# Optimization experiments

Hardware: AMD Instinct MI355X
Metric: run time of the kernel (lower is better)

## Reference

```python
import jax, jax.numpy as jnp
import numpy as np

EMBED_DIM = 512
NUM_HEADS = 8
HEAD_DIM = EMBED_DIM // NUM_HEADS
ATTN_STD = 1.0          # attn_param for attn_type='normal'
# attn_position='center' => no displacement of query indices


def setup_inputs() -> dict:
    key = jax.random.key(0)
    k1, k2, k3 = jax.random.split(key, 3)
    B, S = 4, 4096
    inputs = jax.random.normal(k1, (B, S, EMBED_DIM), dtype=jnp.float32)
    # xavier-uniform-like scale for [E, E] weights
    bound = np.float32(np.sqrt(6.0 / (EMBED_DIM + EMBED_DIM)))
    input_weights = jax.random.uniform(k2, (EMBED_DIM, EMBED_DIM), jnp.float32, -bound, bound)
    output_weight = jax.random.uniform(k3, (EMBED_DIM, EMBED_DIM), jnp.float32, -bound, bound)
    return {"inputs": inputs, "input_weights": input_weights, "output_weight": output_weight}


def _gaussian_weights(s_q, s_v, dtype):
    # logits[i, j] = 1/(std*sqrt(2*pi)) * exp(-0.5*((j-i)/std)^2)
    iq = jnp.arange(s_q, dtype=dtype)[:, None]
    iv = jnp.arange(s_v, dtype=dtype)[None, :]
    diff = iv - iq
    coef = (1.0 / (ATTN_STD * np.sqrt(2.0 * np.pi))).astype(np.float32)
    return coef * jnp.exp(-0.5 * (diff / ATTN_STD) ** 2)


def reference(inputs, input_weights, output_weight):
    B, S, E = inputs.shape
    H, D = NUM_HEADS, HEAD_DIM
    # project(): F.linear(inputs, input_weights) then split heads -> [B*H, S, D]
    v = jnp.einsum('bse,fe->bsf', inputs, input_weights)
    v = v.reshape(B, S, H, D).transpose(0, 2, 1, 3).reshape(B * H, S, D)
    # hard-coded Gaussian positional attention weights [S, S] (data independent)
    w = _gaussian_weights(S, S, inputs.dtype).astype(v.dtype)
    attended = jnp.einsum('qk,nkd->nqd', w, v)  # bmm with broadcast weights
    attended = attended.reshape(B, H, S, D).transpose(0, 2, 1, 3).reshape(B, S, E)
    # output_projection: Linear(E, E, bias=False)
    return jnp.einsum('bse,fe->bsf', attended, output_weight)
```

## Files before the change

### kernel.cpp

```cpp
#include <hip/hip_runtime.h>
#include <hip/hip_bf16.h>


typedef unsigned short u16;
typedef unsigned int u32;
typedef unsigned long long u64;
typedef __attribute__((ext_vector_type(8))) short bf16x8;
typedef __attribute__((ext_vector_type(8))) unsigned short u16x8;
typedef __attribute__((ext_vector_type(4))) float f32x4;
typedef __attribute__((ext_vector_type(2))) u32 u32x2;

typedef __attribute__((address_space(1))) const void* as1_cvp;
typedef __attribute__((address_space(3))) void* as3_vp;

#define EDIM 512
#define NROW 16384
#define NCONVB 4096
#define GOUT 512

__device__ __forceinline__ float b2f(u16 x) {
  union { u32 u; float f; } c; c.u = ((u32)x) << 16; return c.f;
}
__device__ __forceinline__ u16 f2b(float x) {
  union { float f; u32 u; } c; c.f = x;
  return (u16)((c.u + 0x7fffu + ((c.u >> 16) & 1u)) >> 16);
}
__device__ __forceinline__ u32 cvtpk(float lo, float hi) {
  u32 r;
  asm("v_cvt_pk_bf16_f32 %0, %1, %2" : "=v"(r) : "v"(lo), "v"(hi));
  return r;
}
__device__ __forceinline__ void async_cp16(const void* g, void* l) {
  __builtin_amdgcn_global_load_lds((as1_cvp)(u64)g, (as3_vp)(u32)(u64)l, 16, 0, 0);
}

__global__ __launch_bounds__(256) void prep(const float* __restrict__ in,
                                            const float* __restrict__ Win,
                                            const float* __restrict__ Wout,
                                            u16* __restrict__ Mm,
                                            u16* __restrict__ Uo) {
  __shared__ u16 plds[17408];
  int bid = (int)blockIdx.x, t = threadIdx.x;
  if (bid < 64) {
    u16* la = plds;
    u16* lbt = plds + 8704;
    int w = t >> 6, l = t & 63, lr = l & 15, lk = l >> 4;
    int f0 = (bid >> 3) * 64, e0 = (bid & 7) * 64;
    int arow = t >> 2, acol = (t & 3) * 32;
    int cq = t >> 3, eo = (t & 7) * 8;
    const float* pA = Wout + (u64)(f0 + arow) * EDIM + acol;
    const float* pB = Win + (u64)(4 * cq) * EDIM + e0 + eo;
    f32x4 a8[8], b8[8];
#pragma unroll
    for (int i = 0; i < 8; ++i) a8[i] = *(const f32x4*)(pA + i * 4);
#pragma unroll
    for (int r = 0; r < 4; ++r) {
      b8[r * 2 + 0] = *(const f32x4*)(pB + r * EDIM);
      b8[r * 2 + 1] = *(const f32x4*)(pB + r * EDIM + 4);
    }
    f32x4 acc[4] = {};
    for (int kt = 0; kt < 4; ++kt) {
#pragma unroll
      for (int i = 0; i < 4; ++i) {
        u16x8 o;
#pragma unroll
        for (int q = 0; q < 4; ++q) { o[q] = f2b(a8[2 * i][q]); o[4 + q] = f2b(a8[2 * i + 1][q]); }
        *(u16x8*)(la + arow * 136 + acol + i * 8) = o;
      }
#pragma unroll
      for (int j = 0; j < 8; ++j) {
        u32x2 p;
        p[0] = cvtpk(b8[0 + (j >> 2)][j & 3], b8[2 + (j >> 2)][j & 3]);
        p[1] = cvtpk(b8[4 + (j >> 2)][j & 3], b8[6 + (j >> 2)][j & 3]);
        *(u32x2*)(lbt + (eo + j) * 136 + 4 * cq) = p;
      }
      asm volatile("s_waitcnt lgkmcnt(0)" ::: "memory");
      __builtin_amdgcn_sched_barrier(0);
      __builtin_amdgcn_s_barrier();
      if (kt < 3) {
        pA += 128; pB += (u64)128 * EDIM;
#pragma unroll
        for (int i = 0; i < 8; ++i) a8[i] = *(const f32x4*)(pA + i * 4);
#pragma unroll
        for (int r = 0; r < 4; ++r) {
          b8[r * 2 + 0] = *(const f32x4*)(pB + r * EDIM);
          b8[r * 2 + 1] = *(const f32x4*)(pB + r * EDIM + 4);
        }
      }
#pragma unroll
      for (int kk = 0; kk < 128; kk += 32) {
        bf16x8 a = *(const bf16x8*)(la + (w * 16 + lr) * 136 + kk + lk * 8);
#pragma unroll
        for (int ni = 0; ni < 4; ++ni) {
          bf16x8 bb = *(const bf16x8*)(lbt + (ni * 16 + lr) * 136 + kk + lk * 8);
          acc[ni] = __builtin_amdgcn_mfma_f32_16x16x32_bf16(a, bb, acc[ni], 0, 0, 0);
        }
      }
      asm volatile("s_waitcnt lgkmcnt(0)" ::: "memory");
      __builtin_amdgcn_sched_barrier(0);
      __builtin_amdgcn_s_barrier();
    }
#pragma unroll
    for (int ni = 0; ni < 4; ++ni)
#pragma unroll
      for (int r = 0; r < 4; ++r)
        Mm[(u64)(f0 + w * 16 + lk * 4 + r) * EDIM + e0 + ni * 16 + lr] = f2b(acc[ni][r]);
  } else {
    const float G[5] = {0.39894228040143270f, 0.24197072451914337f,
                        0.053990966513188063f, 0.0044318484119380075f,
                        1.3383022576488537e-4f};
    int gid = (bid - 64) * 256 + t;
    int r = gid >> 6, c = (gid & 63) * 8;
    int s = r & 4095;
    const float* base = in + (u64)r * EDIM + c;
    float a[8] = {0.f, 0.f, 0.f, 0.f, 0.f, 0.f, 0.f, 0.f};
#pragma unroll
    for (int d = -4; d <= 4; ++d) {
      if ((unsigned)(s + d) < 4096u) {
        f32x4 v0 = *(const f32x4*)(base + (long)d * EDIM);
        f32x4 v1 = *(const f32x4*)(base + (long)d * EDIM + 4);
        float g = G[d < 0 ? -d : d];
#pragma unroll
        for (int q = 0; q < 4; ++q) { a[q] += g * v0[q]; a[4 + q] += g * v1[q]; }
      }
    }
    u16x8 o;
#pragma unroll
    for (int q = 0; q < 8; ++q) o[q] = f2b(a[q]);
    *(u16x8*)(Uo + (u64)r * EDIM + c) = o;
  }
}

__global__ __launch_bounds__(256) void gemm_out(const u16* __restrict__ U,
                                                const u16* __restrict__ Mm,
                                                float* __restrict__ out) {
  __shared__ u16 lds[32768];
  int t = threadIdx.x;
  int l = t & 63, lr = l & 15, lk = l >> 4;
  int wv = t >> 6, wr = wv >> 1, wc = wv & 1;
  int b = (int)blockIdx.x;
  int wg = (b & 7) * 64 + (b >> 3);
  int m0 = (wg >> 2) * 128;
  int n0 = (wg & 3) * 128;

  int soct = (t & 7) ^ ((t >> 3) & 7);
  const u16* gA = U + (u64)(m0 + (t >> 3)) * EDIM + soct * 8;
  const u16* gB = Mm + (u64)(n0 + (t >> 3)) * EDIM + soct * 8;

  int ard[4], aswz[4], brd[4], bswz[4];
#pragma unroll
  for (int mi = 0; mi < 4; ++mi) {
    int rA = wr * 64 + mi * 16 + lr;
    ard[mi] = rA * 64; aswz[mi] = (rA & 7) << 3;
  }
#pragma unroll
  for (int ni = 0; ni < 4; ++ni) {
    int rB = wc * 64 + ni * 16 + lr;
    brd[ni] = rB * 64; bswz[ni] = (rB & 7) << 3;
  }

  f32x4 acc[4][4] = {};

#pragma unroll
  for (int i = 0; i < 4; ++i) async_cp16(gA + (u64)i * 32 * EDIM, lds + t * 8 + i * 2048);
#pragma unroll
  for (int i = 0; i < 4; ++i) async_cp16(gB + (u64)i * 32 * EDIM, lds + 16384 + t * 8 + i * 2048);

#pragma unroll
  for (int kt = 0; kt < 8; ++kt) {
    asm volatile("s_waitcnt vmcnt(0)" ::: "memory");
    __builtin_amdgcn_sched_barrier(0);
    __builtin_amdgcn_s_barrier();
    if (kt < 7) {
      int ko = (kt + 1) * 64;
      int ab = ((kt + 1) & 1) * 8192, bb = 16384 + ((kt + 1) & 1) * 8192;
#pragma unroll
      for (int i = 0; i < 4; ++i) async_cp16(gA + ko + (u64)i * 32 * EDIM, lds + ab + t * 8 + i * 2048);
#pragma unroll
      for (int i = 0; i < 4; ++i) async_cp16(gB + ko + (u64)i * 32 * EDIM, lds + bb + t * 8 + i * 2048);
    }
    __builtin_amdgcn_sched_barrier(0);
    int ab = (kt & 1) * 8192, bb = 16384 + (kt & 1) * 8192;
#pragma unroll
    for (int kk = 0; kk < 64; kk += 32) {
      bf16x8 af[4], bv[4];
#pragma unroll
      for (int mi = 0; mi < 4; ++mi)
        af[mi] = *(const bf16x8*)(lds + ab + ard[mi] + ((kk + lk * 8) ^ aswz[mi]));
#pragma unroll
      for (int ni = 0; ni < 4; ++ni)
        bv[ni] = *(const bf16x8*)(lds + bb + brd[ni] + ((kk + lk * 8) ^ bswz[ni]));
#pragma unroll
      for (int mi = 0; mi < 4; ++mi)
#pragma unroll
        for (int ni = 0; ni < 4; ++ni)
          acc[mi][ni] = __builtin_amdgcn_mfma_f32_16x16x32_bf16(af[mi], bv[ni],
                                                                acc[mi][ni], 0, 0, 0);
    }
  }

#pragma unroll
  for (int mi = 0; mi < 4; ++mi)
#pragma unroll
    for (int ni = 0; ni < 4; ++ni)
#pragma unroll
      for (int rr = 0; rr < 4; ++rr)
        out[(u64)(m0 + wr * 64 + mi * 16 + lk * 4 + rr) * EDIM +
            n0 + wc * 64 + ni * 16 + lr] = acc[mi][ni][rr];
}

extern "C" void kernel_launch(void* const* d_in, const int* in_sizes, int n_in,
                              void* d_out, int out_size, void* d_ws, size_t ws_size,
                              hipStream_t stream) {
  const float* in   = (const float*)d_in[0];
  const float* Win  = (const float*)d_in[1];
  const float* Wout = (const float*)d_in[2];
  float* outp = (float*)d_out;

  u16* Mm = (u16*)d_ws;
  u16* Uo = (u16*)d_ws + (u64)EDIM * EDIM;

  hipLaunchKernelGGL(prep,     dim3(64 + NCONVB), dim3(256), 0, stream, in, Win, Wout, Mm, Uo);
  hipLaunchKernelGGL(gemm_out, dim3(GOUT),        dim3(256), 0, stream, Uo, Mm, outp);
}
```

Baseline: 39.89 us.

## Fuse Gaussian convolution into output GEMM A-tile loading

Removes the separate convolution pass that wrote a bf16 intermediate U to workspace. The GEMM kernel now loads fp32 input rows (a 16-row halo per 8-row group), applies the 9-tap Gaussian in registers and writes the A tile to LDS, prefetching the next K slice during the MFMA work. The combined-weight GEMM becomes its own small kernel. The intermediate write and read go away, but each of the four N-column blocks re-reads fp32 input with halo redundancy and does more VALU work, and it adds register pressure under launch_bounds(256,2).

```diff
diff --git a/kernel.cpp b/kernel.cpp
--- a/kernel.cpp
+++ b/kernel.cpp
@@ -15,12 +15,7 @@
 
 #define EDIM 512
 #define NROW 16384
-#define NCONVB 4096
-#define GOUT 512
-
-__device__ __forceinline__ float b2f(u16 x) {
-  union { u32 u; float f; } c; c.u = ((u32)x) << 16; return c.f;
-}
+
 __device__ __forceinline__ u16 f2b(float x) {
   union { float f; u32 u; } c; c.f = x;
   return (u16)((c.u + 0x7fffu + ((c.u >> 16) & 1u)) >> 16);
@@ -34,179 +29,221 @@
   __builtin_amdgcn_global_load_lds((as1_cvp)(u64)g, (as3_vp)(u32)(u64)l, 16, 0, 0);
 }
 
-__global__ __launch_bounds__(256) void prep(const float* __restrict__ in,
-                                            const float* __restrict__ Win,
-                                            const float* __restrict__ Wout,
-                                            u16* __restrict__ Mm,
-                                            u16* __restrict__ Uo) {
+__global__ __launch_bounds__(256) void gemm_m(const float* __restrict__ Wout,
+                                              const float* __restrict__ Win,
+                                              u16* __restrict__ Mm) {
   __shared__ u16 plds[17408];
-  int bid = (int)blockIdx.x, t = threadIdx.x;
-  if (bid < 64) {
-    u16* la = plds;
-    u16* lbt = plds + 8704;
-    int w = t >> 6, l = t & 63, lr = l & 15, lk = l >> 4;
-    int f0 = (bid >> 3) * 64, e0 = (bid & 7) * 64;
-    int arow = t >> 2, acol = (t & 3) * 32;
-    int cq = t >> 3, eo = (t & 7) * 8;
-    const float* pA = Wout + (u64)(f0 + arow) * EDIM + acol;
-    const float* pB = Win + (u64)(4 * cq) * EDIM + e0 + eo;
-    f32x4 a8[8], b8[8];
-#pragma unroll
-    for (int i = 0; i < 8; ++i) a8[i] = *(const f32x4*)(pA + i * 4);
-#pragma unroll
-    for (int r = 0; r < 4; ++r) {
-      b8[r * 2 + 0] = *(const f32x4*)(pB + r * EDIM);
-      b8[r * 2 + 1] = *(const f32x4*)(pB + r * EDIM + 4);
-    }
-    f32x4 acc[4] = {};
-    for (int kt = 0; kt < 4; ++kt) {
-#pragma unroll
-      for (int i = 0; i < 4; ++i) {
-        u16x8 o;
-#pragma unroll
-        for (int q = 0; q < 4; ++q) { o[q] = f2b(a8[2 * i][q]); o[4 + q] = f2b(a8[2 * i + 1][q]); }
-        *(u16x8*)(la + arow * 136 + acol + i * 8) = o;
-      }
-#pragma unroll
-      for (int j = 0; j < 8; ++j) {
-        u32x2 p;
-        p[0] = cvtpk(b8[0 + (j >> 2)][j & 3], b8[2 + (j >> 2)][j & 3]);
-        p[1] = cvtpk(b8[4 + (j >> 2)][j & 3], b8[6 + (j >> 2)][j & 3]);
-        *(u32x2*)(lbt + (eo + j) * 136 + 4 * cq) = p;
-      }
+  int t = threadIdx.x;
+  u16* la = plds;
+  u16* lbt = plds + 8704;
+  int w = t >> 6, l = t & 63, lr = l & 15, lk = l >> 4;
+  int f0 = ((int)blockIdx.x >> 3) * 64, e0 = ((int)blockIdx.x & 7) * 64;
+  int arow = t >> 2, acol = (t & 3) * 32;
+  int cq = t >> 3, eo = (t & 7) * 8;
+  const float* pA = Wout + (u64)(f0 + arow) * EDIM + acol;
+  const float* pB = Win + (u64)(4 * cq) * EDIM + e0 + eo;
+  f32x4 a8[8], b8[8];
+#pragma unroll
+  for (int i = 0; i < 8; ++i) a8[i] = *(const f32x4*)(pA + i * 4);
+#pragma unroll
+  for (int r = 0; r < 4; ++r) {
+    b8[r * 2 + 0] = *(const f32x4*)(pB + r * EDIM);
+    b8[r * 2 + 1] = *(const f32x4*)(pB + r * EDIM + 4);
+  }
+  f32x4 acc[4] = {};
+  for (int kt = 0; kt < 4; ++kt) {
+#pragma unroll
+    for (int i = 0; i < 4; ++i) {
+      u16x8 o;
+#pragma unroll
+      for (int q = 0; q < 4; ++q) { o[q] = f2b(a8[2 * i][q]); o[4 + q] = f2b(a8[2 * i + 1][q]); }
+      *(u16x8*)(la + arow * 136 + acol + i * 8) = o;
+    }
+#pragma unroll
+    for (int j = 0; j < 8; ++j) {
+      u32x2 p;
+      p[0] = cvtpk(b8[0 + (j >> 2)][j & 3], b8[2 + (j >> 2)][j & 3]);
+      p[1] = cvtpk(b8[4 + (j >> 2)][j & 3], b8[6 + (j >> 2)][j & 3]);
+      *(u32x2*)(lbt + (eo + j) * 136 + 4 * cq) = p;
+    }
+    asm volatile("s_waitcnt lgkmcnt(0)" ::: "memory");
+    __builtin_amdgcn_sched_barrier(0);
+    __builtin_amdgcn_s_barrier();
+    if (kt < 3) {
+      pA += 128; pB += (u64)128 * EDIM;
+#pragma unroll
+      for (int i = 0; i < 8; ++i) a8[i] = *(const f32x4*)(pA + i * 4);
+#pragma unroll
+      for (int r = 0; r < 4; ++r) {
+        b8[r * 2 + 0] = *(const f32x4*)(pB + r * EDIM);
+        b8[r * 2 + 1] = *(const f32x4*)(pB + r * EDIM + 4);
+      }
+    }
+#pragma unroll
+    for (int kk = 0; kk < 128; kk += 32) {
+      bf16x8 a = *(const bf16x8*)(la + (w * 16 + lr) * 136 + kk + lk * 8);
+#pragma unroll
+      for (int ni = 0; ni < 4; ++ni) {
+        bf16x8 bb = *(const bf16x8*)(lbt + (ni * 16 + lr) * 136 + kk + lk * 8);
+        acc[ni] = __builtin_amdgcn_mfma_f32_16x16x32_bf16(a, bb, acc[ni], 0, 0, 0);
+      }
+    }
+    asm volatile("s_waitcnt lgkmcnt(0)" ::: "memory");
+    __builtin_amdgcn_sched_barrier(0);
+    __builtin_amdgcn_s_barrier();
+  }
+#pragma unroll
+  for (int ni = 0; ni < 4; ++ni)
+#pragma unroll
+    for (int r = 0; r < 4; ++r)
+      Mm[(u64)(f0 + w * 16 + lk * 4 + r) * EDIM + e0 + ni * 16 + lr] = f2b(acc[ni][r]);
+}
+
+template <bool EDGE>
+__device__ __forceinline__ void conv_to_lds(u16* lds, int abase, const f32x4* w,
+                                            int r0, int tg, int ct, const float* G) {
+#pragma unroll
+  for (int j = 0; j < 8; ++j) {
+    f32x4 o = {};
+    if (EDGE) {
+      int rj = r0 + j, bat = rj >> 12;
+#pragma unroll
+      for (int k = 0; k < 9; ++k) {
+        float g = (((rj + k - 4) >> 12) == bat) ? G[k < 4 ? 4 - k : k - 4] : 0.0f;
+#pragma unroll
+        for (int q = 0; q < 4; ++q) o[q] += g * w[j + k][q];
+      }
+    } else {
+#pragma unroll
+      for (int k = 0; k < 9; ++k) {
+        float g = G[k < 4 ? 4 - k : k - 4];
+#pragma unroll
+        for (int q = 0; q < 4; ++q) o[q] += g * w[j + k][q];
+      }
+    }
+    int row = tg * 8 + j;
+    u32x2 p;
+    p[0] = cvtpk(o[0], o[1]);
+    p[1] = cvtpk(o[2], o[3]);
+    *(u32x2*)(lds + abase + ((row * 64 + ct * 4) ^ ((row & 7) << 3))) = p;
+  }
+}
+
+template <bool EDGE>
+__device__ __forceinline__ void fused_body(const float* __restrict__ in,
+                                           const u16* __restrict__ Mm,
+                                           float* __restrict__ out,
+                                           u16* lds, int t, int m0, int n0) {
+  const float G[5] = {0.39894228040143270f, 0.24197072451914337f,
+                      0.053990966513188063f, 0.0044318484119380075f,
+                      1.3383022576488537e-4f};
+  int l = t & 63, lr = l & 15, lk = l >> 4;
+  int wvi = t >> 6, wr = wvi >> 1, wc = wvi & 1;
+  int ct = t & 15, tg = t >> 4;
+  int r0 = m0 + tg * 8;
+
+  u32 woff[16];
+#pragma unroll
+  for (int i = 0; i < 16; ++i) {
+    int rr = r0 - 4 + i;
+    rr = rr < 0 ? 0 : (rr > NROW - 1 ? NROW - 1 : rr);
+    woff[i] = (u32)rr * EDIM + ct * 4;
+  }
+  int soct = (t & 7) ^ ((t >> 3) & 7);
+  const u16* gB = Mm + (u64)(n0 + (t >> 3)) * EDIM + soct * 8;
+
+  int ard[4], aswz[4], brd[4], bswz[4];
+#pragma unroll
+  for (int mi = 0; mi < 4; ++mi) {
+    int rA = wr * 64 + mi * 16 + lr;
+    ard[mi] = rA * 64; aswz[mi] = (rA & 7) << 3;
+  }
+#pragma unroll
+  for (int ni = 0; ni < 4; ++ni) {
+    int rB = wc * 64 + ni * 16 + lr;
+    brd[ni] = rB * 64; bswz[ni] = (rB & 7) << 3;
+  }
+
+  f32x4 acc[4][4] = {};
+  f32x4 w[16];
+
+#pragma unroll
+  for (int i = 0; i < 16; ++i) w[i] = *(const f32x4*)(in + woff[i]);
+  conv_to_lds<EDGE>(lds, 0, w, r0, tg, ct, G);
+#pragma unroll
+  for (int i = 0; i < 4; ++i)
+    async_cp16(gB + (u64)i * 32 * EDIM, lds + 16384 + t * 8 + i * 2048);
+  asm volatile("s_waitcnt lgkmcnt(0)" ::: "memory");
+  __builtin_amdgcn_sched_barrier(0);
+
+#pragma unroll
+  for (int kt = 0; kt < 8; ++kt) {
+    asm volatile("s_waitcnt vmcnt(0)" ::: "memory");
+    __builtin_amdgcn_sched_barrier(0);
+    __builtin_amdgcn_s_barrier();
+    if (kt < 7) {
+#pragma unroll
+      for (int i = 0; i < 16; ++i)
+        w[i] = *(const f32x4*)(in + woff[i] + (kt + 1) * 64);
+    }
+    __builtin_amdgcn_sched_barrier(0);
+    if (kt < 7) {
+#pragma unroll
+      for (int i = 0; i < 4; ++i)
+        async_cp16(gB + (kt + 1) * 64 + (u64)i * 32 * EDIM,
+                   lds + 16384 + ((kt + 1) & 1) * 8192 + t * 8 + i * 2048);
+    }
+    __builtin_amdgcn_sched_barrier(0);
+    int ab = (kt & 1) * 8192, bb = 16384 + (kt & 1) * 8192;
+#pragma unroll
+    for (int kk = 0; kk < 64; kk += 32) {
+      bf16x8 af[4], bv[4];
+#pragma unroll
+      for (int mi = 0; mi < 4; ++mi)
+        af[mi] = *(const bf16x8*)(lds + ab + ard[mi] + ((kk + lk * 8) ^ aswz[mi]));
+#pragma unroll
+      for (int ni = 0; ni < 4; ++ni)
+        bv[ni] = *(const bf16x8*)(lds + bb + brd[ni] + ((kk + lk * 8) ^ bswz[ni]));
+#pragma unroll
+      for (int mi = 0; mi < 4; ++mi)
+#pragma unroll
+        for (int ni = 0; ni < 4; ++ni)
+          acc[mi][ni] = __builtin_amdgcn_mfma_f32_16x16x32_bf16(af[mi], bv[ni],
+                                                                acc[mi][ni], 0, 0, 0);
+    }
+    if (kt < 7) {
+      asm volatile("s_waitcnt vmcnt(4)" ::: "memory");
+      __builtin_amdgcn_sched_barrier(0);
+      conv_to_lds<EDGE>(lds, ((kt + 1) & 1) * 8192, w, r0, tg, ct, G);
       asm volatile("s_waitcnt lgkmcnt(0)" ::: "memory");
       __builtin_amdgcn_sched_barrier(0);
-      __builtin_amdgcn_s_barrier();
-      if (kt < 3) {
-        pA += 128; pB += (u64)128 * EDIM;
-#pragma unroll
-        for (int i = 0; i < 8; ++i) a8[i] = *(const f32x4*)(pA + i * 4);
-#pragma unroll
-        for (int r = 0; r < 4; ++r) {
-          b8[r * 2 + 0] = *(const f32x4*)(pB + r * EDIM);
-          b8[r * 2 + 1] = *(const f32x4*)(pB + r * EDIM + 4);
-        }
-      }
-#pragma unroll
-      for (int kk = 0; kk < 128; kk += 32) {
-        bf16x8 a = *(const bf16x8*)(la + (w * 16 + lr) * 136 + kk + lk * 8);
-#pragma unroll
-        for (int ni = 0; ni < 4; ++ni) {
-          bf16x8 bb = *(const bf16x8*)(lbt + (ni * 16 + lr) * 136 + kk + lk * 8);
-          acc[ni] = __builtin_amdgcn_mfma_f32_16x16x32_bf16(a, bb, acc[ni], 0, 0, 0);
-        }
-      }
-      asm volatile("s_waitcnt lgkmcnt(0)" ::: "memory");
-      __builtin_amdgcn_sched_barrier(0);
-      __builtin_amdgcn_s_barrier();
-    }
+    }
+  }
+
+#pragma unroll
+  for (int mi = 0; mi < 4; ++mi)
 #pragma unroll
     for (int ni = 0; ni < 4; ++ni)
 #pragma unroll
-      for (int r = 0; r < 4; ++r)
-        Mm[(u64)(f0 + w * 16 + lk * 4 + r) * EDIM + e0 + ni * 16 + lr] = f2b(acc[ni][r]);
-  } else {
-    const float G[5] = {0.39894228040143270f, 0.24197072451914337f,
-                        0.053990966513188063f, 0.0044318484119380075f,
-                        1.3383022576488537e-4f};
-    int gid = (bid - 64) * 256 + t;
-    int r = gid >> 6, c = (gid & 63) * 8;
-    int s = r & 4095;
-    const float* base = in + (u64)r * EDIM + c;
-    float a[8] = {0.f, 0.f, 0.f, 0.f, 0.f, 0.f, 0.f, 0.f};
-#pragma unroll
-    for (int d = -4; d <= 4; ++d) {
-      if ((unsigned)(s + d) < 4096u) {
-        f32x4 v0 = *(const f32x4*)(base + (long)d * EDIM);
-        f32x4 v1 = *(const f32x4*)(base + (long)d * EDIM + 4);
-        float g = G[d < 0 ? -d : d];
-#pragma unroll
-        for (int q = 0; q < 4; ++q) { a[q] += g * v0[q]; a[4 + q] += g * v1[q]; }
-      }
-    }
-    u16x8 o;
-#pragma unroll
-    for (int q = 0; q < 8; ++q) o[q] = f2b(a[q]);
-    *(u16x8*)(Uo + (u64)r * EDIM + c) = o;
-  }
-}
-
-__global__ __launch_bounds__(256) void gemm_out(const u16* __restrict__ U,
-                                                const u16* __restrict__ Mm,
-                                                float* __restrict__ out) {
+      for (int rr = 0; rr < 4; ++rr)
+        out[(u64)(m0 + wr * 64 + mi * 16 + lk * 4 + rr) * EDIM +
+            n0 + wc * 64 + ni * 16 + lr] = acc[mi][ni][rr];
+}
+
+__global__ __launch_bounds__(256, 2) void fused_gc(const float* __restrict__ in,
+                                                   const u16* __restrict__ Mm,
+                                                   float* __restrict__ out) {
   __shared__ u16 lds[32768];
   int t = threadIdx.x;
-  int l = t & 63, lr = l & 15, lk = l >> 4;
-  int wv = t >> 6, wr = wv >> 1, wc = wv & 1;
   int b = (int)blockIdx.x;
   int wg = (b & 7) * 64 + (b >> 3);
   int m0 = (wg >> 2) * 128;
   int n0 = (wg & 3) * 128;
-
-  int soct = (t & 7) ^ ((t >> 3) & 7);
-  const u16* gA = U + (u64)(m0 + (t >> 3)) * EDIM + soct * 8;
-  const u16* gB = Mm + (u64)(n0 + (t >> 3)) * EDIM + soct * 8;
-
-  int ard[4], aswz[4], brd[4], bswz[4];
-#pragma unroll
-  for (int mi = 0; mi < 4; ++mi) {
-    int rA = wr * 64 + mi * 16 + lr;
-    ard[mi] = rA * 64; aswz[mi] = (rA & 7) << 3;
-  }
-#pragma unroll
-  for (int ni = 0; ni < 4; ++ni) {
-    int rB = wc * 64 + ni * 16 + lr;
-    brd[ni] = rB * 64; bswz[ni] = (rB & 7) << 3;
-  }
-
-  f32x4 acc[4][4] = {};
-
-#pragma unroll
-  for (int i = 0; i < 4; ++i) async_cp16(gA + (u64)i * 32 * EDIM, lds + t * 8 + i * 2048);
-#pragma unroll
-  for (int i = 0; i < 4; ++i) async_cp16(gB + (u64)i * 32 * EDIM, lds + 16384 + t * 8 + i * 2048);
-
-#pragma unroll
-  for (int kt = 0; kt < 8; ++kt) {
-    asm volatile("s_waitcnt vmcnt(0)" ::: "memory");
-    __builtin_amdgcn_sched_barrier(0);
-    __builtin_amdgcn_s_barrier();
-    if (kt < 7) {
-      int ko = (kt + 1) * 64;
-      int ab = ((kt + 1) & 1) * 8192, bb = 16384 + ((kt + 1) & 1) * 8192;
-#pragma unroll
-      for (int i = 0; i < 4; ++i) async_cp16(gA + ko + (u64)i * 32 * EDIM, lds + ab + t * 8 + i * 2048);
-#pragma unroll
-      for (int i = 0; i < 4; ++i) async_cp16(gB + ko + (u64)i * 32 * EDIM, lds + bb + t * 8 + i * 2048);
-    }
-    __builtin_amdgcn_sched_barrier(0);
-    int ab = (kt & 1) * 8192, bb = 16384 + (kt & 1) * 8192;
-#pragma unroll
-    for (int kk = 0; kk < 64; kk += 32) {
-      bf16x8 af[4], bv[4];
-#pragma unroll
-      for (int mi = 0; mi < 4; ++mi)
-        af[mi] = *(const bf16x8*)(lds + ab + ard[mi] + ((kk + lk * 8) ^ aswz[mi]));
-#pragma unroll
-      for (int ni = 0; ni < 4; ++ni)
-        bv[ni] = *(const bf16x8*)(lds + bb + brd[ni] + ((kk + lk * 8) ^ bswz[ni]));
-#pragma unroll
-      for (int mi = 0; mi < 4; ++mi)
-#pragma unroll
-        for (int ni = 0; ni < 4; ++ni)
-          acc[mi][ni] = __builtin_amdgcn_mfma_f32_16x16x32_bf16(af[mi], bv[ni],
-                                                                acc[mi][ni], 0, 0, 0);
-    }
-  }
-
-#pragma unroll
-  for (int mi = 0; mi < 4; ++mi)
-#pragma unroll
-    for (int ni = 0; ni < 4; ++ni)
-#pragma unroll
-      for (int rr = 0; rr < 4; ++rr)
-        out[(u64)(m0 + wr * 64 + mi * 16 + lk * 4 + rr) * EDIM +
-            n0 + wc * 64 + ni * 16 + lr] = acc[mi][ni][rr];
+  bool edge = (((m0 - 4) >> 12) != ((m0 + 131) >> 12));
+  if (edge)
+    fused_body<true>(in, Mm, out, lds, t, m0, n0);
+  else
+    fused_body<false>(in, Mm, out, lds, t, m0, n0);
 }
 
 extern "C" void kernel_launch(void* const* d_in, const int* in_sizes, int n_in,
@@ -218,8 +255,7 @@
   float* outp = (float*)d_out;
 
   u16* Mm = (u16*)d_ws;
-  u16* Uo = (u16*)d_ws + (u64)EDIM * EDIM;
-
-  hipLaunchKernelGGL(prep,     dim3(64 + NCONVB), dim3(256), 0, stream, in, Win, Wout, Mm, Uo);
-  hipLaunchKernelGGL(gemm_out, dim3(GOUT),        dim3(256), 0, stream, Uo, Mm, outp);
-}
+
+  hipLaunchKernelGGL(gemm_m,   dim3(64),  dim3(256), 0, stream, Wout, Win, Mm);
+  hipLaunchKernelGGL(fused_gc, dim3(512), dim3(256), 0, stream, in, Mm, outp);
+}
```

After: 44.11 us. 1.11x slower.

## Tile conv rows per thread for reuse and triple-buffer A in output GEMM

Applied to the files above, without the earlier changes.

The Gaussian conv stage now has each thread load a 20-row window of float4 columns and produce 12 output rows. This reuses each loaded row across up to 9 taps instead of reloading it per output row, and it uses far fewer blocks, with a separate edge path for batch boundaries. The output GEMM now triple-buffers the A tile and issues its loads two K-steps ahead, waiting only on partial vmcnt, so memory traffic overlaps with the MFMAs. It also adds launch_bounds occupancy 2. The cost is more LDS (80KB) and higher register pressure in both kernels.

```diff
diff --git a/kernel.cpp b/kernel.cpp
--- a/kernel.cpp
+++ b/kernel.cpp
@@ -15,12 +15,10 @@
 
 #define EDIM 512
 #define NROW 16384
-#define NCONVB 4096
+#define CROWS 24
+#define NCONVB 683
 #define GOUT 512
 
-__device__ __forceinline__ float b2f(u16 x) {
-  union { u32 u; float f; } c; c.u = ((u32)x) << 16; return c.f;
-}
 __device__ __forceinline__ u16 f2b(float x) {
   union { float f; u32 u; } c; c.f = x;
   return (u16)((c.u + 0x7fffu + ((c.u >> 16) & 1u)) >> 16);
@@ -32,6 +30,48 @@
 }
 __device__ __forceinline__ void async_cp16(const void* g, void* l) {
   __builtin_amdgcn_global_load_lds((as1_cvp)(u64)g, (as3_vp)(u32)(u64)l, 16, 0, 0);
+}
+
+template <bool EDGE>
+__device__ __forceinline__ void conv_body(const float* __restrict__ in,
+                                          u16* __restrict__ Uo, int cb, int t) {
+  const float G[5] = {0.39894228040143270f, 0.24197072451914337f,
+                      0.053990966513188063f, 0.0044318484119380075f,
+                      1.3383022576488537e-4f};
+  int colv = t & 127;
+  int rgrp = t >> 7;
+  int r0 = cb * CROWS + rgrp * 12;
+  f32x4 w[20];
+  if (EDGE) {
+#pragma unroll
+    for (int i = 0; i < 20; ++i) {
+      int rr = r0 - 4 + i;
+      rr = rr < 0 ? 0 : (rr > NROW - 1 ? NROW - 1 : rr);
+      w[i] = *(const f32x4*)(in + (u64)rr * EDIM + colv * 4);
+    }
+  } else {
+    const float* bp = in + (u64)(r0 - 4) * EDIM + colv * 4;
+#pragma unroll
+    for (int i = 0; i < 20; ++i) w[i] = *(const f32x4*)(bp + (u64)i * EDIM);
+  }
+#pragma unroll
+  for (int j = 0; j < 12; ++j) {
+    int rg = r0 + j;
+    f32x4 o = {};
+#pragma unroll
+    for (int k = 0; k < 9; ++k) {
+      float g = G[k < 4 ? 4 - k : k - 4];
+      if (EDGE) g = (((rg + k - 4) >> 12) == (rg >> 12)) ? g : 0.0f;
+#pragma unroll
+      for (int q = 0; q < 4; ++q) o[q] += g * w[j + k][q];
+    }
+    if (!EDGE || rg < NROW) {
+      u32x2 p;
+      p[0] = cvtpk(o[0], o[1]);
+      p[1] = cvtpk(o[2], o[3]);
+      *(u32x2*)(Uo + (u64)rg * EDIM + colv * 4) = p;
+    }
+  }
 }
 
 __global__ __launch_bounds__(256) void prep(const float* __restrict__ in,
@@ -41,100 +81,119 @@
                                             u16* __restrict__ Uo) {
   __shared__ u16 plds[17408];
   int bid = (int)blockIdx.x, t = threadIdx.x;
-  if (bid < 64) {
-    u16* la = plds;
-    u16* lbt = plds + 8704;
-    int w = t >> 6, l = t & 63, lr = l & 15, lk = l >> 4;
-    int f0 = (bid >> 3) * 64, e0 = (bid & 7) * 64;
-    int arow = t >> 2, acol = (t & 3) * 32;
-    int cq = t >> 3, eo = (t & 7) * 8;
-    const float* pA = Wout + (u64)(f0 + arow) * EDIM + acol;
-    const float* pB = Win + (u64)(4 * cq) * EDIM + e0 + eo;
-    f32x4 a8[8], b8[8];
-#pragma unroll
-    for (int i = 0; i < 8; ++i) a8[i] = *(const f32x4*)(pA + i * 4);
-#pragma unroll
-    for (int r = 0; r < 4; ++r) {
-      b8[r * 2 + 0] = *(const f32x4*)(pB + r * EDIM);
-      b8[r * 2 + 1] = *(const f32x4*)(pB + r * EDIM + 4);
-    }
-    f32x4 acc[4] = {};
-    for (int kt = 0; kt < 4; ++kt) {
-#pragma unroll
-      for (int i = 0; i < 4; ++i) {
-        u16x8 o;
-#pragma unroll
-        for (int q = 0; q < 4; ++q) { o[q] = f2b(a8[2 * i][q]); o[4 + q] = f2b(a8[2 * i + 1][q]); }
-        *(u16x8*)(la + arow * 136 + acol + i * 8) = o;
+  if (bid >= 64) {
+    int cb = bid - 64;
+    int c0 = cb * CROWS;
+    bool edge = (((c0 - 4) >> 12) != ((c0 + CROWS + 3) >> 12));
+    if (edge)
+      conv_body<true>(in, Uo, cb, t);
+    else
+      conv_body<false>(in, Uo, cb, t);
+    return;
+  }
+  u16* la = plds;
+  u16* lbt = plds + 8704;
+  int w = t >> 6, l = t & 63, lr = l & 15, lk = l >> 4;
+  int f0 = (bid >> 3) * 64, e0 = (bid & 7) * 64;
+  int arow = t >> 2, acol = (t & 3) * 32;
+  int cq = t >> 3, eo = (t & 7) * 8;
+  const float* pA = Wout + (u64)(f0 + arow) * EDIM + acol;
+  const float* pB = Win + (u64)(4 * cq) * EDIM + e0 + eo;
+  f32x4 a8[8], b8[8];
+#pragma unroll
+  for (int i = 0; i < 8; ++i) a8[i] = *(const f32x4*)(pA + i * 4);
+#pragma unroll
+  for (int r = 0; r < 4; ++r) {
+    b8[r * 2 + 0] = *(const f32x4*)(pB + r * EDIM);
+    b8[r * 2 + 1] = *(const f32x4*)(pB + r * EDIM + 4);
+  }
+  f32x4 acc[4] = {};
+  for (int kt = 0; kt < 4; ++kt) {
+#pragma unroll
+    for (int i = 0; i < 4; ++i) {
+      u16x8 o;
+#pragma unroll
+      for (int q = 0; q < 4; ++q) { o[q] = f2b(a8[2 * i][q]); o[4 + q] = f2b(a8[2 * i + 1][q]); }
+      *(u16x8*)(la + arow * 136 + acol + i * 8) = o;
+    }
+#pragma unroll
+    for (int j = 0; j < 8; ++j) {
+      u32x2 p;
+      p[0] = cvtpk(b8[0 + (j >> 2)][j & 3], b8[2 + (j >> 2)][j & 3]);
+      p[1] = cvtpk(b8[4 + (j >> 2)][j & 3], b8[6 + (j >> 2)][j & 3]);
+      *(u32x2*)(lbt + (eo + j) * 136 + 4 * cq) = p;
+    }
+    asm volatile("s_waitcnt lgkmcnt(0)" ::: "memory");
+    __builtin_amdgcn_sched_barrier(0);
+    __builtin_amdgcn_s_barrier();
+    if (kt < 3) {
+      pA += 128; pB += (u64)128 * EDIM;
+#pragma unroll
+      for (int i = 0; i < 8; ++i) a8[i] = *(const f32x4*)(pA + i * 4);
+#pragma unroll
+      for (int r = 0; r < 4; ++r) {
+        b8[r * 2 + 0] = *(const f32x4*)(pB + r * EDIM);
+        b8[r * 2 + 1] = *(const f32x4*)(pB + r * EDIM + 4);
       }
-#pragma unroll
-      for (int j = 0; j < 8; ++j) {
-        u32x2 p;
-        p[0] = cvtpk(b8[0 + (j >> 2)][j & 3], b8[2 + (j >> 2)][j & 3]);
-        p[1] = cvtpk(b8[4 + (j >> 2)][j & 3], b8[6 + (j >> 2)][j & 3]);
-        *(u32x2*)(lbt + (eo + j) * 136 + 4 * cq) = p;
+    }
+#pragma unroll
+    for (int kk = 0; kk < 128; kk += 32) {
+      bf16x8 a = *(const bf16x8*)(la + (w * 16 + lr) * 136 + kk + lk * 8);
+#pragma unroll
+      for (int ni = 0; ni < 4; ++ni) {
+        bf16x8 bb = *(const bf16x8*)(lbt + (ni * 16 + lr) * 136 + kk + lk * 8);
+        acc[ni] = __builtin_amdgcn_mfma_f32_16x16x32_bf16(a, bb, acc[ni], 0, 0, 0);
       }
-      asm volatile("s_waitcnt lgkmcnt(0)" ::: "memory");
-      __builtin_amdgcn_sched_barrier(0);
-      __builtin_amdgcn_s_barrier();
-      if (kt < 3) {
-        pA += 128; pB += (u64)128 * EDIM;
-#pragma unroll
-        for (int i = 0; i < 8; ++i) a8[i] = *(const f32x4*)(pA + i * 4);
-#pragma unroll
-        for (int r = 0; r < 4; ++r) {
-          b8[r * 2 + 0] = *(const f32x4*)(pB + r * EDIM);
-          b8[r * 2 + 1] = *(const f32x4*)(pB + r * EDIM + 4);
-        }
-      }
-#pragma unroll
-      for (int kk = 0; kk < 128; kk += 32) {
-        bf16x8 a = *(const bf16x8*)(la + (w * 16 + lr) * 136 + kk + lk * 8);
-#pragma unroll
-        for (int ni = 0; ni < 4; ++ni) {
-          bf16x8 bb = *(const bf16x8*)(lbt + (ni * 16 + lr) * 136 + kk + lk * 8);
-          acc[ni] = __builtin_amdgcn_mfma_f32_16x16x32_bf16(a, bb, acc[ni], 0, 0, 0);
-        }
-      }
-      asm volatile("s_waitcnt lgkmcnt(0)" ::: "memory");
-      __builtin_amdgcn_sched_barrier(0);
-      __builtin_amdgcn_s_barrier();
-    }
-#pragma unroll
-    for (int ni = 0; ni < 4; ++ni)
-#pragma unroll
-      for (int r = 0; r < 4; ++r)
-        Mm[(u64)(f0 + w * 16 + lk * 4 + r) * EDIM + e0 + ni * 16 + lr] = f2b(acc[ni][r]);
-  } else {
-    const float G[5] = {0.39894228040143270f, 0.24197072451914337f,
-                        0.053990966513188063f, 0.0044318484119380075f,
-                        1.3383022576488537e-4f};
-    int gid = (bid - 64) * 256 + t;
-    int r = gid >> 6, c = (gid & 63) * 8;
-    int s = r & 4095;
-    const float* base = in + (u64)r * EDIM + c;
-    float a[8] = {0.f, 0.f, 0.f, 0.f, 0.f, 0.f, 0.f, 0.f};
-#pragma unroll
-    for (int d = -4; d <= 4; ++d) {
-      if ((unsigned)(s + d) < 4096u) {
-        f32x4 v0 = *(const f32x4*)(base + (long)d * EDIM);
-        f32x4 v1 = *(const f32x4*)(base + (long)d * EDIM + 4);
-        float g = G[d < 0 ? -d : d];
-#pragma unroll
-        for (int q = 0; q < 4; ++q) { a[q] += g * v0[q]; a[4 + q] += g * v1[q]; }
-      }
-    }
-    u16x8 o;
-#pragma unroll
-    for (int q = 0; q < 8; ++q) o[q] = f2b(a[q]);
-    *(u16x8*)(Uo + (u64)r * EDIM + c) = o;
-  }
-}
-
-__global__ __launch_bounds__(256) void gemm_out(const u16* __restrict__ U,
-                                                const u16* __restrict__ Mm,
-                                                float* __restrict__ out) {
-  __shared__ u16 lds[32768];
+    }
+    asm volatile("s_waitcnt lgkmcnt(0)" ::: "memory");
+    __builtin_amdgcn_sched_barrier(0);
+    __builtin_amdgcn_s_barrier();
+  }
+#pragma unroll
+  for (int ni = 0; ni < 4; ++ni)
+#pragma unroll
+    for (int r = 0; r < 4; ++r)
+      Mm[(u64)(f0 + w * 16 + lk * 4 + r) * EDIM + e0 + ni * 16 + lr] = f2b(acc[ni][r]);
+}
+
+#define ISSA(KT, BUF)                                                          \
+  _Pragma("unroll") for (int i = 0; i < 4; ++i)                                \
+      async_cp16(gA + (KT) * 64 + (u64)i * 32 * EDIM,                          \
+                 lds + (BUF) + t * 8 + i * 2048);
+#define ISSB(KT, BUF)                                                          \
+  _Pragma("unroll") for (int i = 0; i < 4; ++i)                                \
+      async_cp16(gB + (KT) * 64 + (u64)i * 32 * EDIM,                          \
+                 lds + 24576 + (BUF) + t * 8 + i * 2048);
+
+#define GSTEP(KT, VM)                                                          \
+  {                                                                            \
+    asm volatile("s_waitcnt vmcnt(" #VM ")" ::: "memory");                     \
+    __builtin_amdgcn_sched_barrier(0);                                         \
+    __builtin_amdgcn_s_barrier();                                              \
+    if ((KT) + 1 < 8) { ISSB((KT) + 1, (((KT) + 1) & 1) * 8192) }              \
+    __builtin_amdgcn_sched_barrier(0);                                         \
+    if ((KT) + 2 < 8) { ISSA((KT) + 2, (((KT) + 2) % 3) * 8192) }              \
+    __builtin_amdgcn_sched_barrier(0);                                         \
+    const int ab = ((KT) % 3) * 8192, bb = 24576 + ((KT) & 1) * 8192;          \
+    _Pragma("unroll") for (int kk = 0; kk < 64; kk += 32) {                    \
+      bf16x8 af[4], bv[4];                                                     \
+      _Pragma("unroll") for (int mi = 0; mi < 4; ++mi)                         \
+          af[mi] = *(const bf16x8*)(lds + ab + ard[mi] +                       \
+                                    ((kk + lk * 8) ^ aswz[mi]));               \
+      _Pragma("unroll") for (int ni = 0; ni < 4; ++ni)                         \
+          bv[ni] = *(const bf16x8*)(lds + bb + brd[ni] +                       \
+                                    ((kk + lk * 8) ^ bswz[ni]));               \
+      _Pragma("unroll") for (int mi = 0; mi < 4; ++mi)                         \
+        _Pragma("unroll") for (int ni = 0; ni < 4; ++ni)                       \
+            acc[mi][ni] = __builtin_amdgcn_mfma_f32_16x16x32_bf16(             \
+                af[mi], bv[ni], acc[mi][ni], 0, 0, 0);                         \
+    }                                                                          \
+  }
+
+__global__ __launch_bounds__(256, 2) void gemm_out(const u16* __restrict__ U,
+                                                   const u16* __restrict__ Mm,
+                                                   float* __restrict__ out) {
+  __shared__ u16 lds[40960];
   int t = threadIdx.x;
   int l = t & 63, lr = l & 15, lk = l >> 4;
   int wv = t >> 6, wr = wv >> 1, wc = wv & 1;
@@ -161,43 +220,14 @@
 
   f32x4 acc[4][4] = {};
 
-#pragma unroll
-  for (int i = 0; i < 4; ++i) async_cp16(gA + (u64)i * 32 * EDIM, lds + t * 8 + i * 2048);
-#pragma unroll
-  for (int i = 0; i < 4; ++i) async_cp16(gB + (u64)i * 32 * EDIM, lds + 16384 + t * 8 + i * 2048);
-
-#pragma unroll
-  for (int kt = 0; kt < 8; ++kt) {
-    asm volatile("s_waitcnt vmcnt(0)" ::: "memory");
-    __builtin_amdgcn_sched_barrier(0);
-    __builtin_amdgcn_s_barrier();
-    if (kt < 7) {
-      int ko = (kt + 1) * 64;
-      int ab = ((kt + 1) & 1) * 8192, bb = 16384 + ((kt + 1) & 1) * 8192;
-#pragma unroll
-      for (int i = 0; i < 4; ++i) async_cp16(gA + ko + (u64)i * 32 * EDIM, lds + ab + t * 8 + i * 2048);
-#pragma unroll
-      for (int i = 0; i < 4; ++i) async_cp16(gB + ko + (u64)i * 32 * EDIM, lds + bb + t * 8 + i * 2048);
-    }
-    __builtin_amdgcn_sched_barrier(0);
-    int ab = (kt & 1) * 8192, bb = 16384 + (kt & 1) * 8192;
-#pragma unroll
-    for (int kk = 0; kk < 64; kk += 32) {
-      bf16x8 af[4], bv[4];
-#pragma unroll
-      for (int mi = 0; mi < 4; ++mi)
-        af[mi] = *(const bf16x8*)(lds + ab + ard[mi] + ((kk + lk * 8) ^ aswz[mi]));
-#pragma unroll
-      for (int ni = 0; ni < 4; ++ni)
-        bv[ni] = *(const bf16x8*)(lds + bb + brd[ni] + ((kk + lk * 8) ^ bswz[ni]));
-#pragma unroll
-      for (int mi = 0; mi < 4; ++mi)
-#pragma unroll
-        for (int ni = 0; ni < 4; ++ni)
-          acc[mi][ni] = __builtin_amdgcn_mfma_f32_16x16x32_bf16(af[mi], bv[ni],
-                                                                acc[mi][ni], 0, 0, 0);
-    }
-  }
+  ISSA(0, 0)
+  ISSB(0, 0)
+  __builtin_amdgcn_sched_barrier(0);
+  ISSA(1, 8192)
+  __builtin_amdgcn_sched_barrier(0);
+
+  GSTEP(0, 4) GSTEP(1, 4) GSTEP(2, 4) GSTEP(3, 4)
+  GSTEP(4, 4) GSTEP(5, 4) GSTEP(6, 4) GSTEP(7, 0)
 
 #pragma unroll
   for (int mi = 0; mi < 4; ++mi)
```

Result: faster. 33.91 us (median of 2 runs) (-15.0%).
